# Kernel tuning notes

Measured on AMD Instinct MI355X. Metric: run time of the kernel, lower is better.

The kernel has to match this reference:

```python
import jax, jax.numpy as jnp
import numpy as np

N = 50000
E = 800000
IN_CH = 128
HID = 16
HEADS = 16
OUT_CH = 64
NEG_SLOPE = 0.2
EPS = 1e-16


def _add_self_loops(edge_index, n):
    loops = jnp.arange(n, dtype=edge_index.dtype)
    src = jnp.concatenate([edge_index[0], loops])
    dst = jnp.concatenate([edge_index[1], loops])
    return src, dst


def gat_conv(x, src, dst, W, a_src, a_dst, b, heads, out_ch, concat, n):
    # x: [N, F_in], W: [F_in, heads*out_ch], a_src/a_dst: [heads, out_ch]
    h = (x @ W).reshape(n, heads, out_ch)                 # [N, H, C]
    alpha_src = jnp.sum(h * a_src, axis=-1)               # [N, H]
    alpha_dst = jnp.sum(h * a_dst, axis=-1)               # [N, H]
    e = alpha_src[src] + alpha_dst[dst]                   # [E, H]
    e = jnp.where(e > 0, e, NEG_SLOPE * e)                # LeakyReLU(0.2)
    m = jax.ops.segment_max(e, dst, num_segments=n)       # [N, H] (finite: self-loops)
    ex = jnp.exp(e - m[dst])                              # [E, H]
    denom = jax.ops.segment_sum(ex, dst, num_segments=n)  # [N, H]
    alpha = ex / (denom[dst] + EPS)                       # [E, H]
    msg = h[src] * alpha[:, :, None]                      # [E, H, C]
    out = jax.ops.segment_sum(msg, dst, num_segments=n)   # [N, H, C]
    if concat:
        out = out.reshape(n, heads * out_ch)
    else:
        out = out.mean(axis=1)
    return out + b


def setup_inputs() -> dict:
    key = jax.random.key(0)
    ks = jax.random.split(key, 10)
    x = jax.random.normal(ks[0], (N, IN_CH), dtype=jnp.float32)
    edge_index = jax.random.randint(ks[1], (2, E), 0, N, dtype=jnp.int64)
    s1 = 1.0 / np.sqrt(IN_CH)
    W1 = jax.random.normal(ks[2], (IN_CH, HEADS * HID), dtype=jnp.float32) * s1
    a_src1 = jax.random.normal(ks[3], (HEADS, HID), dtype=jnp.float32) * (1.0 / np.sqrt(HID))
    a_dst1 = jax.random.normal(ks[4], (HEADS, HID), dtype=jnp.float32) * (1.0 / np.sqrt(HID))
    b1 = jnp.zeros((HEADS * HID,), dtype=jnp.float32)
    s2 = 1.0 / np.sqrt(HEADS * HID)
    W2 = jax.random.normal(ks[5], (HEADS * HID, OUT_CH), dtype=jnp.float32) * s2
    a_src2 = jax.random.normal(ks[6], (1, OUT_CH), dtype=jnp.float32) * (1.0 / np.sqrt(OUT_CH))
    a_dst2 = jax.random.normal(ks[7], (1, OUT_CH), dtype=jnp.float32) * (1.0 / np.sqrt(OUT_CH))
    b2 = jnp.zeros((OUT_CH,), dtype=jnp.float32)
    return {"x": x, "edge_index": edge_index, "W1": W1, "a_src1": a_src1,
            "a_dst1": a_dst1, "b1": b1, "W2": W2, "a_src2": a_src2,
            "a_dst2": a_dst2, "b2": b2}


def reference(x, edge_index, W1, a_src1, a_dst1, b1, W2, a_src2, a_dst2, b2):
    src, dst = _add_self_loops(edge_index, N)
    h = gat_conv(x, src, dst, W1, a_src1, a_dst1, b1, HEADS, HID, True, N)
    h = gat_conv(h, src, dst, W2, a_src2, a_dst2, b2, 1, OUT_CH, False, N)
    return jax.nn.sigmoid(h)
```

## Files before the change

### kernel.cpp

```cpp
#include <hip/hip_runtime.h>
#include <hip/hip_bf16.h>

#define NN 50000
#define EE 800000
#define TE 850000
#define BK 64

typedef __hip_bfloat16 bf16;
typedef __attribute__((ext_vector_type(8))) short short8v;
typedef __attribute__((ext_vector_type(4))) float float4v;

__device__ __forceinline__ float bu2f(unsigned short v) {
    return __uint_as_float((unsigned)v << 16);
}
__device__ __forceinline__ unsigned short f2bu(float v) {
    bf16 t = __float2bfloat16(v);
    return *(unsigned short*)&t;
}
__device__ __forceinline__ float lrelu(float e) { return (e > 0.f) ? e : 0.2f * e; }
__device__ __forceinline__ int clampn(int v) {
    return (v < 0) ? 0 : (v >= NN ? NN - 1 : v);
}

__device__ __forceinline__ int block_isi64(const void* ei) {
    __shared__ int sflag;
    int t = threadIdx.x;
    if (t < 64) {
        unsigned z = (((const unsigned*)ei)[2 * t + 1] == 0u) ? 1u : 0u;
        unsigned long long m = __ballot(z);
        if (t == 0) sflag = (__popcll(m) >= 32) ? 1 : 0;
    }
    __syncthreads();
    return sflag;
}

__global__ void prep_k(const void* __restrict__ ei, int* __restrict__ deg,
                       int* __restrict__ csr,
                       const float* __restrict__ W1, const float* __restrict__ W2,
                       const float* __restrict__ asr1, const float* __restrict__ ads1,
                       const float* __restrict__ asr2, const float* __restrict__ ads2,
                       unsigned short* __restrict__ W1T,
                       unsigned short* __restrict__ W2T,
                       unsigned short* __restrict__ P1sT,
                       unsigned short* __restrict__ P1dT,
                       unsigned short* __restrict__ P2T) {
    int isi64 = block_isi64(ei);
    int b = blockIdx.x, t = threadIdx.x;
    if (b < 128) {
        int j = b * 256 + t;
        int n = j >> 7, k = j & 127;
        W1T[j] = f2bu(W1[k * 256 + n]);
    } else if (b < 192) {
        int j = (b - 128) * 256 + t;
        int n = j >> 8, k = j & 255;
        W2T[j] = f2bu(W2[k * 64 + n]);
    } else if (b == 192) {
        for (int j = t; j < 2048; j += 256) {
            int h = j >> 7, k = j & 127;
            float s = 0.f, d = 0.f;
            for (int c = 0; c < 16; ++c) {
                float wv = W1[k * 256 + h * 16 + c];
                s += wv * asr1[h * 16 + c];
                d += wv * ads1[h * 16 + c];
            }
            P1sT[j] = f2bu(s);
            P1dT[j] = f2bu(d);
        }
    } else if (b == 193) {
        int k = t;
        float s = 0.f, d = 0.f;
        for (int c = 0; c < 64; ++c) {
            float wv = W2[k * 64 + c];
            s += wv * asr2[c];
            d += wv * ads2[c];
        }
        P2T[k] = f2bu(s);
        P2T[256 + k] = f2bu(d);
        for (int j = 512 + t; j < 4096; j += 256) P2T[j] = 0;
    }
    int p = b * 256 + t;
    int i0 = p * 2;
    if (i0 >= TE) return;
    int s0, d0, s1 = -1, d1 = -1;
    if (i0 + 1 < EE) {
        if (isi64) {
            longlong2 sv = ((const longlong2*)ei)[p];
            longlong2 dv = ((const longlong2*)ei)[(EE >> 1) + p];
            s0 = clampn((int)sv.x); s1 = clampn((int)sv.y);
            d0 = clampn((int)dv.x); d1 = clampn((int)dv.y);
        } else {
            int2 sv = ((const int2*)ei)[p];
            int2 dv = ((const int2*)ei)[(EE >> 1) + p];
            s0 = clampn(sv.x); s1 = clampn(sv.y);
            d0 = clampn(dv.x); d1 = clampn(dv.y);
        }
    } else {
        auto lde = [&](long long idx) {
            return clampn(isi64 ? (int)((const long long*)ei)[idx] : ((const int*)ei)[idx]);
        };
        if (i0 < EE) { s0 = lde(i0); d0 = lde((long long)EE + i0); }
        else         { s0 = i0 - EE; d0 = i0 - EE; }
        if (i0 + 1 < TE) {
            if (i0 + 1 < EE) { s1 = lde(i0 + 1); d1 = lde((long long)EE + i0 + 1); }
            else             { s1 = i0 + 1 - EE; d1 = i0 + 1 - EE; }
        }
    }
    int pos0 = atomicAdd(&deg[d0], 1);
    if (pos0 < BK) csr[d0 * BK + pos0] = s0;
    if (d1 >= 0) {
        int pos1 = atomicAdd(&deg[d1], 1);
        if (pos1 < BK) csr[d1 * BK + pos1] = s1;
    }
}

__global__ __launch_bounds__(256) void gemm1_k(
    const float* __restrict__ x, const unsigned short* __restrict__ W1T,
    const unsigned short* __restrict__ P1sT, const unsigned short* __restrict__ P1dT,
    bf16* __restrict__ h1, float* __restrict__ a_src, float* __restrict__ a_dst) {
    int wv = threadIdx.x >> 6, lane = threadIdx.x & 63;
    int m = lane & 15, quad = lane >> 4;
    int row0 = blockIdx.x * 64 + wv * 16;
    int arow = row0 + m;
    int arowc = (arow < NN) ? arow : NN - 1;
    const float4* x4 = (const float4*)x;
    short8v a[4];
#pragma unroll
    for (int ks = 0; ks < 4; ++ks) {
        float4 f0 = x4[(size_t)arowc * 32 + ks * 8 + quad * 2];
        float4 f1 = x4[(size_t)arowc * 32 + ks * 8 + quad * 2 + 1];
        union { short8v v; unsigned short u[8]; } ua;
        ua.u[0] = f2bu(f0.x); ua.u[1] = f2bu(f0.y);
        ua.u[2] = f2bu(f0.z); ua.u[3] = f2bu(f0.w);
        ua.u[4] = f2bu(f1.x); ua.u[5] = f2bu(f1.y);
        ua.u[6] = f2bu(f1.z); ua.u[7] = f2bu(f1.w);
        a[ks] = ua.v;
    }
    float4v accs = {0.f, 0.f, 0.f, 0.f}, accd = {0.f, 0.f, 0.f, 0.f};
#pragma unroll
    for (int ks = 0; ks < 4; ++ks) {
        short8v bs = *(const short8v*)&P1sT[(size_t)m * 128 + quad * 8 + ks * 32];
        short8v bd = *(const short8v*)&P1dT[(size_t)m * 128 + quad * 8 + ks * 32];
        accs = __builtin_amdgcn_mfma_f32_16x16x32_bf16(a[ks], bs, accs, 0, 0, 0);
        accd = __builtin_amdgcn_mfma_f32_16x16x32_bf16(a[ks], bd, accd, 0, 0, 0);
    }
    float4v acc[16];
#pragma unroll
    for (int t = 0; t < 16; ++t) {
        float4v c = {0.f, 0.f, 0.f, 0.f};
        const unsigned short* wb = &W1T[(size_t)(t * 16 + m) * 128 + quad * 8];
#pragma unroll
        for (int ks = 0; ks < 4; ++ks) {
            short8v b = *(const short8v*)&wb[ks * 32];
            c = __builtin_amdgcn_mfma_f32_16x16x32_bf16(a[ks], b, c, 0, 0, 0);
        }
        acc[t] = c;
    }
#pragma unroll
    for (int t = 0; t < 16; ++t) {
#pragma unroll
        for (int r = 0; r < 4; ++r) {
            int orow = row0 + quad * 4 + r;
            if (orow < NN)
                h1[(size_t)orow * 256 + t * 16 + m] = __float2bfloat16(acc[t][r]);
        }
    }
#pragma unroll
    for (int r = 0; r < 4; ++r) {
        int orow = row0 + quad * 4 + r;
        if (orow < NN) {
            a_src[orow * 16 + m] = accs[r];
            a_dst[orow * 16 + m] = accd[r];
        }
    }
}

__global__ __launch_bounds__(256) void agg1f_k(
    const int* __restrict__ deg, int* __restrict__ csr,
    const float* __restrict__ a_src, const float* __restrict__ a_dst,
    const bf16* __restrict__ h1, const float* __restrict__ b1,
    const unsigned short* __restrict__ W2T, const unsigned short* __restrict__ P2T,
    bf16* __restrict__ h2, float* __restrict__ a_src2, float* __restrict__ a_dst2) {
    __shared__ int sbuf[4][64];
    __shared__ unsigned short sout[4][272];
    int wv = threadIdx.x >> 6, lane = threadIdx.x & 63;
    int dst = blockIdx.x * 4 + wv;
    int d = deg[dst]; if (d > BK) d = BK;
    int base = dst * BK;
    int v = (lane < d) ? csr[base + lane] : 0x7fffffff;
    int rank = 0;
    for (int j = 0; j < d; ++j) {
        int vj = __shfl(v, j, 64);
        rank += (vj < v || (vj == v && j < lane)) ? 1 : 0;
    }
    if (lane < d) sbuf[wv][rank] = v;
    if (lane < d) csr[base + lane] = sbuf[wv][lane];
    int we = lane >> 4, wh = lane & 15;
    int hc = lane >> 2;
    float adst_w = a_dst[dst * 16 + wh];
    float ax = 0.f, ay = 0.f, az = 0.f, aw = 0.f;
    float dsum = 0.f;
    int t0 = 0;
    for (; t0 + 4 <= d; t0 += 4) {
        int sr = sbuf[wv][t0 + we];
        float wr = __expf(lrelu(a_src[sr * 16 + wh] + adst_w));
        dsum += wr;
#pragma unroll
        for (int j = 0; j < 4; ++j) {
            float wj = __shfl(wr, j * 16 + hc, 64);
            int sj = sbuf[wv][t0 + j];
            ushort4 hv = *(const ushort4*)&h1[(size_t)sj * 256 + lane * 4];
            ax += wj * bu2f(hv.x);
            ay += wj * bu2f(hv.y);
            az += wj * bu2f(hv.z);
            aw += wj * bu2f(hv.w);
        }
    }
    if (t0 < d) {
        int n = d - t0;
        float wr = 0.f;
        if (we < n) {
            int sr = sbuf[wv][t0 + we];
            wr = __expf(lrelu(a_src[sr * 16 + wh] + adst_w));
        }
        dsum += wr;
        for (int j = 0; j < n; ++j) {
            float wj = __shfl(wr, j * 16 + hc, 64);
            int sj = sbuf[wv][t0 + j];
            ushort4 hv = *(const ushort4*)&h1[(size_t)sj * 256 + lane * 4];
            ax += wj * bu2f(hv.x);
            ay += wj * bu2f(hv.y);
            az += wj * bu2f(hv.z);
            aw += wj * bu2f(hv.w);
        }
    }
    dsum += __shfl_xor(dsum, 16, 64);
    dsum += __shfl_xor(dsum, 32, 64);
    float invd = 1.f / (__shfl(dsum, hc, 64) + 1e-16f);
    float4 bv = *(const float4*)&b1[lane * 4];
    ushort4 st;
    st.x = f2bu(ax * invd + bv.x);
    st.y = f2bu(ay * invd + bv.y);
    st.z = f2bu(az * invd + bv.z);
    st.w = f2bu(aw * invd + bv.w);
    *(ushort4*)&sout[wv][lane * 4] = st;
    __syncthreads();
    {
        int mm = lane & 15, qq = lane >> 4;
        short8v a2[8];
#pragma unroll
        for (int ks = 0; ks < 8; ++ks)
            a2[ks] = *(const short8v*)&sout[mm & 3][ks * 32 + qq * 8];
        float4v c2 = {0.f, 0.f, 0.f, 0.f};
        const unsigned short* wb2 = &W2T[(size_t)(wv * 16 + mm) * 256 + qq * 8];
#pragma unroll
        for (int ks = 0; ks < 8; ++ks) {
            short8v b = *(const short8v*)&wb2[ks * 32];
            c2 = __builtin_amdgcn_mfma_f32_16x16x32_bf16(a2[ks], b, c2, 0, 0, 0);
        }
        if (qq == 0) {
#pragma unroll
            for (int r = 0; r < 4; ++r)
                h2[(size_t)(blockIdx.x * 4 + r) * 64 + wv * 16 + mm] =
                    __float2bfloat16(c2[r]);
        }
        if (wv == 0) {
            float4v ca = {0.f, 0.f, 0.f, 0.f};
            const unsigned short* pb = &P2T[(size_t)mm * 256 + qq * 8];
#pragma unroll
            for (int ks = 0; ks < 8; ++ks) {
                short8v b = *(const short8v*)&pb[ks * 32];
                ca = __builtin_amdgcn_mfma_f32_16x16x32_bf16(a2[ks], b, ca, 0, 0, 0);
            }
            if (qq == 0 && mm == 0) {
#pragma unroll
                for (int r = 0; r < 4; ++r) a_src2[blockIdx.x * 4 + r] = ca[r];
            }
            if (qq == 0 && mm == 1) {
#pragma unroll
                for (int r = 0; r < 4; ++r) a_dst2[blockIdx.x * 4 + r] = ca[r];
            }
        }
    }
}

__global__ __launch_bounds__(256) void agg2_k(
    const int* __restrict__ deg, const int* __restrict__ csr,
    const float* __restrict__ a_src2, const float* __restrict__ a_dst2,
    const bf16* __restrict__ h2, const float* __restrict__ b2,
    float* __restrict__ out) {
    int wv = threadIdx.x >> 6;
    int lane = threadIdx.x & 63;
    int dst = blockIdx.x * 4 + wv;
    if (dst >= NN) return;
    int d = deg[dst]; if (d > BK) d = BK;
    int base = dst * BK;
    float adst = a_dst2[dst];
    int half = lane >> 5, hl = lane & 31;
    float acc0 = 0.f, acc1 = 0.f, dsum = 0.f;
    float wr = 0.f; int sr = 0;
    if (lane < d) {
        sr = csr[base + lane];
        wr = __expf(lrelu(a_src2[sr] + adst));
    }
    dsum += wr;
    for (int j0 = 0; j0 < d; j0 += 8) {
        ushort2 hv[4];
        float wj[4];
#pragma unroll
        for (int u = 0; u < 4; ++u) {
            int j = j0 + u * 2 + half;
            int jc = (j < d) ? j : 0;
            float w = __shfl(wr, jc, 64);
            int sj = __shfl(sr, jc, 64);
            wj[u] = (j < d) ? w : 0.f;
            hv[u] = *(const ushort2*)&h2[(size_t)sj * 64 + hl * 2];
        }
#pragma unroll
        for (int u = 0; u < 4; ++u) {
            acc0 += wj[u] * bu2f(hv[u].x);
            acc1 += wj[u] * bu2f(hv[u].y);
        }
    }
    acc0 += __shfl_xor(acc0, 32, 64);
    acc1 += __shfl_xor(acc1, 32, 64);
#pragma unroll
    for (int o = 32; o >= 1; o >>= 1) dsum += __shfl_xor(dsum, o, 64);
    if (half == 0) {
        float inv = 1.f / (dsum + 1e-16f);
        float o0 = acc0 * inv + b2[hl * 2];
        float o1 = acc1 * inv + b2[hl * 2 + 1];
        float2 st;
        st.x = 1.f / (1.f + __expf(-o0));
        st.y = 1.f / (1.f + __expf(-o1));
        *(float2*)&out[(size_t)dst * 64 + hl * 2] = st;
    }
}


extern "C" void kernel_launch(void* const* d_in, const int* in_sizes, int n_in,
                              void* d_out, int out_size, void* d_ws, size_t ws_size,
                              hipStream_t stream) {
    const float* x    = (const float*)d_in[0];
    const void*  ei   = d_in[1];
    const float* W1   = (const float*)d_in[2];
    const float* asr1 = (const float*)d_in[3];
    const float* ads1 = (const float*)d_in[4];
    const float* b1   = (const float*)d_in[5];
    const float* W2   = (const float*)d_in[6];
    const float* asr2 = (const float*)d_in[7];
    const float* ads2 = (const float*)d_in[8];
    const float* b2   = (const float*)d_in[9];
    float* out = (float*)d_out;

    char* w = (char*)d_ws;
    auto carve = [&](size_t bytes) {
        void* p = (void*)w;
        w += (bytes + 255) & ~(size_t)255;
        return p;
    };
    int*    csr      = (int*)carve((size_t)NN * BK * 4);
    int*    deg      = (int*)carve((size_t)NN * 4);
    float*  a_src1   = (float*)carve((size_t)NN * 16 * 4);
    float*  a_dst1   = (float*)carve((size_t)NN * 16 * 4);
    unsigned short* W1T  = (unsigned short*)carve(128 * 256 * 2);
    unsigned short* W2T  = (unsigned short*)carve(256 * 64 * 2);
    unsigned short* P1sT = (unsigned short*)carve(16 * 128 * 2);
    unsigned short* P1dT = (unsigned short*)carve(16 * 128 * 2);
    unsigned short* P2T  = (unsigned short*)carve(16 * 256 * 2);
    bf16*   h1       = (bf16*)carve((size_t)NN * 256 * 2);
    bf16*   h2       = (bf16*)carve((size_t)NN * 64 * 2);
    float*  a_src2   = (float*)carve((size_t)NN * 4);
    float*  a_dst2   = (float*)carve((size_t)NN * 4);

    hipMemsetAsync(deg, 0, (size_t)NN * 4, stream);

    const int pgrid = ((TE + 1) / 2 + 255) / 256;
    prep_k<<<pgrid, 256, 0, stream>>>(ei, deg, csr, W1, W2, asr1, ads1, asr2, ads2,
                                      W1T, W2T, P1sT, P1dT, P2T);
    gemm1_k<<<(NN + 63) / 64, 256, 0, stream>>>(x, W1T, P1sT, P1dT, h1, a_src1, a_dst1);
    agg1f_k<<<NN / 4, 256, 0, stream>>>(deg, csr, a_src1, a_dst1, h1, b1,
                                        W2T, P2T, h2, a_src2, a_dst2);
    agg2_k<<<(NN + 3) / 4, 256, 0, stream>>>(deg, csr, a_src2, a_dst2, h2, b2, out);
}
```

Measured before the change: 302.0 us.

## Fuse edge CSR build with layer-1 GEMM, drop memset, per-wave layer-2 projection

Replaces the memset plus combined prep kernel with a small weight-prep kernel that also zeroes the degree array. The edge bucketing and the layer-1 GEMM now run as separate block ranges of one launch so they can overlap. The layer-2 projection in the aggregation kernel no longer syncs the whole block: each wave computes all 64 outputs for its own destination, using only one useful row of each MFMA. This removes a launch and a barrier, in exchange for redundant MFMA work per wave.

```diff
diff --git a/kernel.cpp b/kernel.cpp
--- a/kernel.cpp
+++ b/kernel.cpp
@@ -5,6 +5,8 @@
 #define EE 800000
 #define TE 850000
 #define BK 64
+#define NGB 782
+#define NEB 1661
 
 typedef __hip_bfloat16 bf16;
 typedef __attribute__((ext_vector_type(8))) short short8v;
@@ -22,30 +24,15 @@
     return (v < 0) ? 0 : (v >= NN ? NN - 1 : v);
 }
 
-__device__ __forceinline__ int block_isi64(const void* ei) {
-    __shared__ int sflag;
-    int t = threadIdx.x;
-    if (t < 64) {
-        unsigned z = (((const unsigned*)ei)[2 * t + 1] == 0u) ? 1u : 0u;
-        unsigned long long m = __ballot(z);
-        if (t == 0) sflag = (__popcll(m) >= 32) ? 1 : 0;
-    }
-    __syncthreads();
-    return sflag;
-}
-
-__global__ void prep_k(const void* __restrict__ ei, int* __restrict__ deg,
-                       int* __restrict__ csr,
-                       const float* __restrict__ W1, const float* __restrict__ W2,
-                       const float* __restrict__ asr1, const float* __restrict__ ads1,
-                       const float* __restrict__ asr2, const float* __restrict__ ads2,
-                       unsigned short* __restrict__ W1T,
-                       unsigned short* __restrict__ W2T,
-                       unsigned short* __restrict__ P1sT,
-                       unsigned short* __restrict__ P1dT,
-                       unsigned short* __restrict__ P2T) {
-    int isi64 = block_isi64(ei);
+__global__ __launch_bounds__(256) void wprep_k(
+    const float* __restrict__ W1, const float* __restrict__ W2,
+    const float* __restrict__ asr1, const float* __restrict__ ads1,
+    const float* __restrict__ asr2, const float* __restrict__ ads2,
+    unsigned short* __restrict__ W1T, unsigned short* __restrict__ W2T,
+    unsigned short* __restrict__ P1sT, unsigned short* __restrict__ P1dT,
+    unsigned short* __restrict__ P2T, int* __restrict__ deg) {
     int b = blockIdx.x, t = threadIdx.x;
+    for (int i = b * 256 + t; i < NN; i += 256 * 256) deg[i] = 0;
     if (b < 128) {
         int j = b * 256 + t;
         int n = j >> 7, k = j & 127;
@@ -78,7 +65,82 @@
         P2T[256 + k] = f2bu(d);
         for (int j = 512 + t; j < 4096; j += 256) P2T[j] = 0;
     }
-    int p = b * 256 + t;
+}
+
+__global__ __launch_bounds__(256) void eg1_k(
+    const void* __restrict__ ei, const float* __restrict__ x,
+    const unsigned short* __restrict__ W1T,
+    const unsigned short* __restrict__ P1sT, const unsigned short* __restrict__ P1dT,
+    int* __restrict__ deg, int* __restrict__ csr,
+    bf16* __restrict__ h1, float* __restrict__ a_src, float* __restrict__ a_dst) {
+    if (blockIdx.x < NGB) {
+        int wv = threadIdx.x >> 6, lane = threadIdx.x & 63;
+        int m = lane & 15, quad = lane >> 4;
+        int row0 = blockIdx.x * 64 + wv * 16;
+        int arow = row0 + m;
+        int arowc = (arow < NN) ? arow : NN - 1;
+        const float4* x4 = (const float4*)x;
+        short8v a[4];
+#pragma unroll
+        for (int ks = 0; ks < 4; ++ks) {
+            float4 f0 = x4[(size_t)arowc * 32 + ks * 8 + quad * 2];
+            float4 f1 = x4[(size_t)arowc * 32 + ks * 8 + quad * 2 + 1];
+            union { short8v v; unsigned short u[8]; } ua;
+            ua.u[0] = f2bu(f0.x); ua.u[1] = f2bu(f0.y);
+            ua.u[2] = f2bu(f0.z); ua.u[3] = f2bu(f0.w);
+            ua.u[4] = f2bu(f1.x); ua.u[5] = f2bu(f1.y);
+            ua.u[6] = f2bu(f1.z); ua.u[7] = f2bu(f1.w);
+            a[ks] = ua.v;
+        }
+        float4v accs = {0.f, 0.f, 0.f, 0.f}, accd = {0.f, 0.f, 0.f, 0.f};
+#pragma unroll
+        for (int ks = 0; ks < 4; ++ks) {
+            short8v bs = *(const short8v*)&P1sT[(size_t)m * 128 + quad * 8 + ks * 32];
+            short8v bd = *(const short8v*)&P1dT[(size_t)m * 128 + quad * 8 + ks * 32];
+            accs = __builtin_amdgcn_mfma_f32_16x16x32_bf16(a[ks], bs, accs, 0, 0, 0);
+            accd = __builtin_amdgcn_mfma_f32_16x16x32_bf16(a[ks], bd, accd, 0, 0, 0);
+        }
+        float4v acc[16];
+#pragma unroll
+        for (int t = 0; t < 16; ++t) {
+            float4v c = {0.f, 0.f, 0.f, 0.f};
+            const unsigned short* wb = &W1T[(size_t)(t * 16 + m) * 128 + quad * 8];
+#pragma unroll
+            for (int ks = 0; ks < 4; ++ks) {
+                short8v b = *(const short8v*)&wb[ks * 32];
+                c = __builtin_amdgcn_mfma_f32_16x16x32_bf16(a[ks], b, c, 0, 0, 0);
+            }
+            acc[t] = c;
+        }
+#pragma unroll
+        for (int t = 0; t < 16; ++t) {
+#pragma unroll
+            for (int r = 0; r < 4; ++r) {
+                int orow = row0 + quad * 4 + r;
+                if (orow < NN)
+                    h1[(size_t)orow * 256 + t * 16 + m] = __float2bfloat16(acc[t][r]);
+            }
+        }
+#pragma unroll
+        for (int r = 0; r < 4; ++r) {
+            int orow = row0 + quad * 4 + r;
+            if (orow < NN) {
+                a_src[orow * 16 + m] = accs[r];
+                a_dst[orow * 16 + m] = accd[r];
+            }
+        }
+        return;
+    }
+    __shared__ int sflag;
+    int t = threadIdx.x;
+    if (t < 64) {
+        unsigned z = (((const unsigned*)ei)[2 * t + 1] == 0u) ? 1u : 0u;
+        unsigned long long mb = __ballot(z);
+        if (t == 0) sflag = (__popcll(mb) >= 32) ? 1 : 0;
+    }
+    __syncthreads();
+    int isi64 = sflag;
+    int p = (blockIdx.x - NGB) * 256 + t;
     int i0 = p * 2;
     if (i0 >= TE) return;
     int s0, d0, s1 = -1, d1 = -1;
@@ -113,68 +175,7 @@
     }
 }
 
-__global__ __launch_bounds__(256) void gemm1_k(
-    const float* __restrict__ x, const unsigned short* __restrict__ W1T,
-    const unsigned short* __restrict__ P1sT, const unsigned short* __restrict__ P1dT,
-    bf16* __restrict__ h1, float* __restrict__ a_src, float* __restrict__ a_dst) {
-    int wv = threadIdx.x >> 6, lane = threadIdx.x & 63;
-    int m = lane & 15, quad = lane >> 4;
-    int row0 = blockIdx.x * 64 + wv * 16;
-    int arow = row0 + m;
-    int arowc = (arow < NN) ? arow : NN - 1;
-    const float4* x4 = (const float4*)x;
-    short8v a[4];
-#pragma unroll
-    for (int ks = 0; ks < 4; ++ks) {
-        float4 f0 = x4[(size_t)arowc * 32 + ks * 8 + quad * 2];
-        float4 f1 = x4[(size_t)arowc * 32 + ks * 8 + quad * 2 + 1];
-        union { short8v v; unsigned short u[8]; } ua;
-        ua.u[0] = f2bu(f0.x); ua.u[1] = f2bu(f0.y);
-        ua.u[2] = f2bu(f0.z); ua.u[3] = f2bu(f0.w);
-        ua.u[4] = f2bu(f1.x); ua.u[5] = f2bu(f1.y);
-        ua.u[6] = f2bu(f1.z); ua.u[7] = f2bu(f1.w);
-        a[ks] = ua.v;
-    }
-    float4v accs = {0.f, 0.f, 0.f, 0.f}, accd = {0.f, 0.f, 0.f, 0.f};
-#pragma unroll
-    for (int ks = 0; ks < 4; ++ks) {
-        short8v bs = *(const short8v*)&P1sT[(size_t)m * 128 + quad * 8 + ks * 32];
-        short8v bd = *(const short8v*)&P1dT[(size_t)m * 128 + quad * 8 + ks * 32];
-        accs = __builtin_amdgcn_mfma_f32_16x16x32_bf16(a[ks], bs, accs, 0, 0, 0);
-        accd = __builtin_amdgcn_mfma_f32_16x16x32_bf16(a[ks], bd, accd, 0, 0, 0);
-    }
-    float4v acc[16];
-#pragma unroll
-    for (int t = 0; t < 16; ++t) {
-        float4v c = {0.f, 0.f, 0.f, 0.f};
-        const unsigned short* wb = &W1T[(size_t)(t * 16 + m) * 128 + quad * 8];
-#pragma unroll
-        for (int ks = 0; ks < 4; ++ks) {
-            short8v b = *(const short8v*)&wb[ks * 32];
-            c = __builtin_amdgcn_mfma_f32_16x16x32_bf16(a[ks], b, c, 0, 0, 0);
-        }
-        acc[t] = c;
-    }
-#pragma unroll
-    for (int t = 0; t < 16; ++t) {
-#pragma unroll
-        for (int r = 0; r < 4; ++r) {
-            int orow = row0 + quad * 4 + r;
-            if (orow < NN)
-                h1[(size_t)orow * 256 + t * 16 + m] = __float2bfloat16(acc[t][r]);
-        }
-    }
-#pragma unroll
-    for (int r = 0; r < 4; ++r) {
-        int orow = row0 + quad * 4 + r;
-        if (orow < NN) {
-            a_src[orow * 16 + m] = accs[r];
-            a_dst[orow * 16 + m] = accd[r];
-        }
-    }
-}
-
-__global__ __launch_bounds__(256) void agg1f_k(
+__global__ __launch_bounds__(256) void agg1m_k(
     const int* __restrict__ deg, int* __restrict__ csr,
     const float* __restrict__ a_src, const float* __restrict__ a_dst,
     const bf16* __restrict__ h1, const float* __restrict__ b1,
@@ -243,43 +244,33 @@
     st.z = f2bu(az * invd + bv.z);
     st.w = f2bu(aw * invd + bv.w);
     *(ushort4*)&sout[wv][lane * 4] = st;
-    __syncthreads();
     {
         int mm = lane & 15, qq = lane >> 4;
         short8v a2[8];
 #pragma unroll
         for (int ks = 0; ks < 8; ++ks)
-            a2[ks] = *(const short8v*)&sout[mm & 3][ks * 32 + qq * 8];
-        float4v c2 = {0.f, 0.f, 0.f, 0.f};
-        const unsigned short* wb2 = &W2T[(size_t)(wv * 16 + mm) * 256 + qq * 8];
+            a2[ks] = *(const short8v*)&sout[wv][ks * 32 + qq * 8];
+#pragma unroll
+        for (int t = 0; t < 4; ++t) {
+            float4v c2 = {0.f, 0.f, 0.f, 0.f};
+            const unsigned short* wb2 = &W2T[(size_t)(t * 16 + mm) * 256 + qq * 8];
+#pragma unroll
+            for (int ks = 0; ks < 8; ++ks) {
+                short8v b = *(const short8v*)&wb2[ks * 32];
+                c2 = __builtin_amdgcn_mfma_f32_16x16x32_bf16(a2[ks], b, c2, 0, 0, 0);
+            }
+            if (qq == 0)
+                h2[(size_t)dst * 64 + t * 16 + mm] = __float2bfloat16(c2[0]);
+        }
+        float4v ca = {0.f, 0.f, 0.f, 0.f};
+        const unsigned short* pb = &P2T[(size_t)mm * 256 + qq * 8];
 #pragma unroll
         for (int ks = 0; ks < 8; ++ks) {
-            short8v b = *(const short8v*)&wb2[ks * 32];
-            c2 = __builtin_amdgcn_mfma_f32_16x16x32_bf16(a2[ks], b, c2, 0, 0, 0);
-        }
-        if (qq == 0) {
-#pragma unroll
-            for (int r = 0; r < 4; ++r)
-                h2[(size_t)(blockIdx.x * 4 + r) * 64 + wv * 16 + mm] =
-                    __float2bfloat16(c2[r]);
-        }
-        if (wv == 0) {
-            float4v ca = {0.f, 0.f, 0.f, 0.f};
-            const unsigned short* pb = &P2T[(size_t)mm * 256 + qq * 8];
-#pragma unroll
-            for (int ks = 0; ks < 8; ++ks) {
-                short8v b = *(const short8v*)&pb[ks * 32];
-                ca = __builtin_amdgcn_mfma_f32_16x16x32_bf16(a2[ks], b, ca, 0, 0, 0);
-            }
-            if (qq == 0 && mm == 0) {
-#pragma unroll
-                for (int r = 0; r < 4; ++r) a_src2[blockIdx.x * 4 + r] = ca[r];
-            }
-            if (qq == 0 && mm == 1) {
-#pragma unroll
-                for (int r = 0; r < 4; ++r) a_dst2[blockIdx.x * 4 + r] = ca[r];
-            }
-        }
+            short8v b = *(const short8v*)&pb[ks * 32];
+            ca = __builtin_amdgcn_mfma_f32_16x16x32_bf16(a2[ks], b, ca, 0, 0, 0);
+        }
+        if (lane == 0) a_src2[dst] = ca[0];
+        if (lane == 1) a_dst2[dst] = ca[0];
     }
 }
 
@@ -372,13 +363,11 @@
     float*  a_src2   = (float*)carve((size_t)NN * 4);
     float*  a_dst2   = (float*)carve((size_t)NN * 4);
 
-    hipMemsetAsync(deg, 0, (size_t)NN * 4, stream);
-
-    const int pgrid = ((TE + 1) / 2 + 255) / 256;
-    prep_k<<<pgrid, 256, 0, stream>>>(ei, deg, csr, W1, W2, asr1, ads1, asr2, ads2,
-                                      W1T, W2T, P1sT, P1dT, P2T);
-    gemm1_k<<<(NN + 63) / 64, 256, 0, stream>>>(x, W1T, P1sT, P1dT, h1, a_src1, a_dst1);
-    agg1f_k<<<NN / 4, 256, 0, stream>>>(deg, csr, a_src1, a_dst1, h1, b1,
+    wprep_k<<<256, 256, 0, stream>>>(W1, W2, asr1, ads1, asr2, ads2,
+                                     W1T, W2T, P1sT, P1dT, P2T, deg);
+    eg1_k<<<NGB + NEB, 256, 0, stream>>>(ei, x, W1T, P1sT, P1dT,
+                                         deg, csr, h1, a_src1, a_dst1);
+    agg1m_k<<<NN / 4, 256, 0, stream>>>(deg, csr, a_src1, a_dst1, h1, b1,
                                         W2T, P2T, h2, a_src2, a_dst2);
     agg2_k<<<(NN + 3) / 4, 256, 0, stream>>>(deg, csr, a_src2, a_dst2, h2, b2, out);
 }
```

Measured after the change: 431.1 us. 1.43x slower.
